# Kernel optimization log

Measured on AMD Instinct MI355X. Metric: run time of the kernel, lower is better.

The kernel has to match this reference:

```python
import jax, jax.numpy as jnp
import numpy as np

B, T, I, H, FF, C = 4096, 512, 13, 7, 512, 1


def setup_inputs() -> dict:
    key = jax.random.key(0)
    ks = jax.random.split(key, 9)
    s_ih = 1.0 / np.sqrt(H)
    return {
        "x": jax.random.normal(ks[0], (B, T, I), dtype=jnp.float32),
        # PyTorch LSTM params, gate order i,f,g,o, uniform(-1/sqrt(H), 1/sqrt(H))
        "w_ih": jax.random.uniform(ks[1], (4 * H, I), minval=-s_ih, maxval=s_ih, dtype=jnp.float32),
        "w_hh": jax.random.uniform(ks[2], (4 * H, H), minval=-s_ih, maxval=s_ih, dtype=jnp.float32),
        "b_ih": jax.random.uniform(ks[3], (4 * H,), minval=-s_ih, maxval=s_ih, dtype=jnp.float32),
        "b_hh": jax.random.uniform(ks[4], (4 * H,), minval=-s_ih, maxval=s_ih, dtype=jnp.float32),
        "fc1_w": jax.random.uniform(ks[5], (FF, H), minval=-s_ih, maxval=s_ih, dtype=jnp.float32),
        "fc1_b": jax.random.uniform(ks[6], (FF,), minval=-s_ih, maxval=s_ih, dtype=jnp.float32),
        "fc_w": jax.random.uniform(ks[7], (C, FF), minval=-1.0 / np.sqrt(FF), maxval=1.0 / np.sqrt(FF), dtype=jnp.float32),
        "fc_b": jax.random.uniform(ks[8], (C,), minval=-1.0 / np.sqrt(FF), maxval=1.0 / np.sqrt(FF), dtype=jnp.float32),
    }


def _lstm_last_hidden(x, w_ih, w_hh, b_ih, b_hh):
    # Precompute input contributions for all timesteps: [B, T, 4H]
    xg = jnp.einsum("bti,gi->btg", x, w_ih) + b_ih

    def step(carry, xg_t):
        h, c = carry
        gates = xg_t + h @ w_hh.T + b_hh  # [B, 4H]
        i, f, g, o = jnp.split(gates, 4, axis=-1)
        i = jax.nn.sigmoid(i)
        f = jax.nn.sigmoid(f)
        g = jnp.tanh(g)
        o = jax.nn.sigmoid(o)
        c = f * c + i * g
        h = o * jnp.tanh(c)
        return (h, c), None

    h0 = jnp.zeros((x.shape[0], w_hh.shape[1]), dtype=x.dtype)
    (hn, _), _ = jax.lax.scan(step, (h0, h0), jnp.swapaxes(xg, 0, 1))
    return hn  # [B, H]


def reference(x, w_ih, w_hh, b_ih, b_hh, fc1_w, fc1_b, fc_w, fc_b):
    # Dropout(0.1) is identity in eval mode.
    hn = _lstm_last_hidden(x, w_ih, w_hh, b_ih, b_hh)
    out = jax.nn.relu(hn)
    out = jax.nn.relu(out @ fc1_w.T + fc1_b)
    return out @ fc_w.T + fc_b  # [B, 1]
```

## Files before the change

kernel.cpp:

```cpp
#include <hip/hip_runtime.h>

#define BB 4096
#define TN 512
#define IN 13
#define HN 7
#define FFD 512
#define CT 16
#define NCK (TN / CT)
#define GPB 2

#define SWZ(v, imm) __int_as_float(__builtin_amdgcn_ds_swizzle(__float_as_int(v), (imm)))
#define QB(v, q)    __int_as_float(__builtin_amdgcn_mov_dpp(__float_as_int(v), (q)*0x55, 0xF, 0xF, true))

__device__ __forceinline__ float2 pkfma(float2 a, float2 b, float2 c) {
    float2 d;
    asm("v_pk_fma_f32 %0, %1, %2, %3" : "=v"(d) : "v"(a), "v"(b), "v"(c));
    return d;
}

__global__ __launch_bounds__(128, 7)
void lstm_fused(const float* __restrict__ x,
                const float* __restrict__ w_ih,
                const float* __restrict__ w_hh,
                const float* __restrict__ b_ih,
                const float* __restrict__ b_hh,
                const float* __restrict__ fc1_w,
                const float* __restrict__ fc1_b,
                const float* __restrict__ fc_w,
                const float* __restrict__ fc_b,
                float* __restrict__ out)
{
    __shared__ float2 xd2[2][CT/2][64];
    __shared__ float  xs[IN][GPB][CT];

    const int tid  = threadIdx.x;
    const int wid  = tid >> 6;
    const int l64  = tid & 63;
    const int grp  = l64 >> 5;
    const int lane = l64 & 31;
    const int b    = blockIdx.x * GPB + grp;

    const int tau = lane & 3;
    const int ju  = lane >> 2;
    const int jj  = (ju < HN) ? ju : (HN - 1);
    const int row = tau * HN + jj;

    const float L2E  = 1.4426950408889634f;
    const bool  is_tanh = (tau == 2);
    const float kmul = is_tanh ? (-2.0f * L2E) : (-L2E);
    const float sc   = is_tanh ?  2.0f : 1.0f;
    const float offc = is_tanh ? -1.0f : 0.0f;

    const int s_st = lane & 15;
    const int h_st = (lane >> 4) & 1;
    const int cb   = h_st * 7;
    float2 w2[IN];
    float2 bias2;
    float  p[7];

    float whh[HN];

    if (wid == 1) {
#pragma unroll
        for (int i = 0; i < IN; ++i) {
            const float w = kmul * w_ih[row * IN + i];
            w2[i] = make_float2(w, w);
        }
        const float bsum = kmul * (b_ih[row] + b_hh[row]);
        bias2 = make_float2(bsum, bsum);
    } else {
#pragma unroll
        for (int k = 0; k < HN; ++k) whh[k] = kmul * w_hh[row * HN + k];
        __builtin_amdgcn_s_setprio(1);
    }

    float h0 = 0.f, h1 = 0.f, h2 = 0.f, h3 = 0.f, h4 = 0.f, h5 = 0.f, h6 = 0.f;
    float cval = 0.0f;

    if (wid == 1) {
        const float* src0 = x + ((long)b * TN + s_st) * IN + cb;
#pragma unroll
        for (int c = 0; c < 6; ++c) p[c] = src0[c];
        if (h_st == 0) p[6] = src0[6];
#pragma unroll
        for (int c = 0; c < 6; ++c) xs[cb + c][grp][s_st] = p[c];
        if (h_st == 0) xs[cb + 6][grp][s_st] = p[6];
        {
            const float* src1 = x + ((long)b * TN + CT + s_st) * IN + cb;
#pragma unroll
            for (int c = 0; c < 6; ++c) p[c] = src1[c];
            if (h_st == 0) p[6] = src1[6];
        }
#pragma unroll
        for (int q = 0; q < CT; q += 4) {
            float2 accA = bias2, accB = bias2;
#pragma unroll
            for (int i = 0; i < IN; ++i) {
                const float4 xv = *(const float4*)&xs[i][grp][q];
                accA = pkfma(w2[i], make_float2(xv.x, xv.y), accA);
                accB = pkfma(w2[i], make_float2(xv.z, xv.w), accB);
            }
            xd2[0][(q >> 1) + 0][l64] = accA;
            xd2[0][(q >> 1) + 1][l64] = accB;
        }
    }
    __syncthreads();

    for (int ck = 0; ck < NCK; ++ck) {
        if (wid == 1) {
            const int nk = ck + 1;
            if (nk < NCK) {
#pragma unroll
                for (int c = 0; c < 6; ++c) xs[cb + c][grp][s_st] = p[c];
                if (h_st == 0) xs[cb + 6][grp][s_st] = p[6];
                if (nk + 1 < NCK) {
                    const float* src = x + ((long)b * TN + (nk + 1) * CT + s_st) * IN + cb;
#pragma unroll
                    for (int c = 0; c < 6; ++c) p[c] = src[c];
                    if (h_st == 0) p[6] = src[6];
                }
                const int buf = nk & 1;
#pragma unroll
                for (int q = 0; q < CT; q += 4) {
                    float2 accA = bias2, accB = bias2;
#pragma unroll
                    for (int i = 0; i < IN; ++i) {
                        const float4 xv = *(const float4*)&xs[i][grp][q];
                        accA = pkfma(w2[i], make_float2(xv.x, xv.y), accA);
                        accB = pkfma(w2[i], make_float2(xv.z, xv.w), accB);
                    }
                    xd2[buf][(q >> 1) + 0][l64] = accA;
                    xd2[buf][(q >> 1) + 1][l64] = accB;
                }
            }
        } else {
            const int buf = ck & 1;
            float xr[CT];
#pragma unroll
            for (int pq = 0; pq < CT / 2; ++pq) {
                const float2 v = xd2[buf][pq][l64];
                xr[2 * pq]     = v.x;
                xr[2 * pq + 1] = v.y;
            }
#pragma unroll
            for (int s = 0; s < CT; ++s) {
                float s0 = fmaf(whh[0], h0, xr[s]);
                s0 = fmaf(whh[1], h1, s0);
                s0 = fmaf(whh[2], h2, s0);
                s0 = fmaf(whh[3], h3, s0);
                float s1 = whh[4] * h4;
                s1 = fmaf(whh[5], h5, s1);
                s1 = fmaf(whh[6], h6, s1);
                const float sg = s0 + s1;

                float e   = __builtin_amdgcn_exp2f(sg);
                float val = fmaf(__builtin_amdgcn_rcpf(1.0f + e), sc, offc);

                const float iv = QB(val, 0);
                const float fv = QB(val, 1);
                const float gv = QB(val, 2);
                const float ov = QB(val, 3);

                cval = fmaf(fv, cval, iv * gv);
                float e2 = __builtin_amdgcn_exp2f(-2.0f * L2E * cval);
                float th = fmaf(__builtin_amdgcn_rcpf(1.0f + e2), 2.0f, -1.0f);
                const float hq = ov * th;

                h0 = SWZ(hq, (0  << 5));
                h1 = SWZ(hq, (4  << 5));
                h2 = SWZ(hq, (8  << 5));
                h3 = SWZ(hq, (12 << 5));
                h4 = SWZ(hq, (16 << 5));
                h5 = SWZ(hq, (20 << 5));
                h6 = SWZ(hq, (24 << 5));
            }
        }
        __syncthreads();
    }

    if (wid == 1) return;

    float hb[HN] = { fmaxf(h0,0.f), fmaxf(h1,0.f), fmaxf(h2,0.f), fmaxf(h3,0.f),
                     fmaxf(h4,0.f), fmaxf(h5,0.f), fmaxf(h6,0.f) };

    float acc = 0.0f;
#pragma unroll
    for (int k = 0; k < FFD / 32; ++k) {
        const int r = lane + (k << 5);
        float s = fc1_b[r];
#pragma unroll
        for (int j = 0; j < HN; ++j) s = fmaf(fc1_w[r * HN + j], hb[j], s);
        s = fmaxf(s, 0.0f);
        acc = fmaf(fc_w[r], s, acc);
    }
#pragma unroll
    for (int o = 16; o >= 1; o >>= 1) acc += __shfl_xor(acc, o, 32);
    if (lane == 0) out[b] = acc + fc_b[0];
}

extern "C" void kernel_launch(void* const* d_in, const int* in_sizes, int n_in,
                              void* d_out, int out_size, void* d_ws, size_t ws_size,
                              hipStream_t stream) {
    const float* x     = (const float*)d_in[0];
    const float* w_ih  = (const float*)d_in[1];
    const float* w_hh  = (const float*)d_in[2];
    const float* b_ih  = (const float*)d_in[3];
    const float* b_hh  = (const float*)d_in[4];
    const float* fc1_w = (const float*)d_in[5];
    const float* fc1_b = (const float*)d_in[6];
    const float* fc_w  = (const float*)d_in[7];
    const float* fc_b  = (const float*)d_in[8];
    float* out = (float*)d_out;

    dim3 grid(BB / GPB);
    dim3 block(128);
    hipLaunchKernelGGL(lstm_fused, grid, block, 0, stream,
                       x, w_ih, w_hh, b_ih, b_hh, fc1_w, fc1_b, fc_w, fc_b, out);
}
```

Before: 105.2 us.

## Replace ds_swizzle hidden-state broadcast with permlane16 swap plus DPP row rotates

The per-step broadcast of the 7 hidden values across lanes moves from seven LDS-crossbar ds_swizzle ops to one v_permlane16_swap and six DPP row_ror moves. The recurrent weights are re-permuted at setup so each lane's rotated operand pairs with the right w_hh column, with zero weights padding the missing 8th slot. This targets the latency of the serial LSTM recurrence, where each step waits on the h exchange. The launch-bounds occupancy hint also drops from 7 to 4, which loosens the register budget but may lower the number of resident waves.

```diff
diff --git a/kernel.cpp b/kernel.cpp
--- a/kernel.cpp
+++ b/kernel.cpp
@@ -9,8 +9,32 @@
 #define NCK (TN / CT)
 #define GPB 2
 
-#define SWZ(v, imm) __int_as_float(__builtin_amdgcn_ds_swizzle(__float_as_int(v), (imm)))
+#if defined(__has_builtin)
+#  if __has_builtin(__builtin_amdgcn_permlane16_swap)
+#    define HAVE_PL16 1
+#  endif
+#endif
+
 #define QB(v, q)    __int_as_float(__builtin_amdgcn_mov_dpp(__float_as_int(v), (q)*0x55, 0xF, 0xF, true))
+#define RORF(v, n)  __int_as_float(__builtin_amdgcn_mov_dpp(__float_as_int(v), 0x120 + (n), 0xF, 0xF, true))
+
+__device__ __forceinline__ void rowswap(float& a, float& b) {
+#ifdef HAVE_PL16
+    auto r = __builtin_amdgcn_permlane16_swap(__float_as_uint(a), __float_as_uint(b),
+                                              false, false);
+    a = __uint_as_float(r[0]);
+    b = __uint_as_float(r[1]);
+#else
+    float ta, tb;
+    asm volatile("v_mov_b32 %0, %2\n"
+                 "v_mov_b32 %1, %3\n"
+                 "s_nop 1\n"
+                 "v_permlane16_swap_b32 %0, %1"
+                 : "=&v"(ta), "=&v"(tb)
+                 : "v"(a), "v"(b));
+    a = ta; b = tb;
+#endif
+}
 
 __device__ __forceinline__ float2 pkfma(float2 a, float2 b, float2 c) {
     float2 d;
@@ -18,7 +42,7 @@
     return d;
 }
 
-__global__ __launch_bounds__(128, 7)
+__global__ __launch_bounds__(128, 4)
 void lstm_fused(const float* __restrict__ x,
                 const float* __restrict__ w_ih,
                 const float* __restrict__ w_hh,
@@ -44,12 +68,21 @@
     const int ju  = lane >> 2;
     const int jj  = (ju < HN) ? ju : (HN - 1);
     const int row = tau * HN + jj;
+    const int jr  = ju & 3;
 
     const float L2E  = 1.4426950408889634f;
     const bool  is_tanh = (tau == 2);
     const float kmul = is_tanh ? (-2.0f * L2E) : (-L2E);
     const float sc   = is_tanh ?  2.0f : 1.0f;
     const float offc = is_tanh ? -1.0f : 0.0f;
+
+    const int pr = __builtin_amdgcn_mov_dpp(l64, 0x124, 0xF, 0xF, true);
+    const bool ror_plus = ((pr & 15) == ((l64 + 4) & 15));
+    float paf = __int_as_float(l64);
+    float pbf = __int_as_float(l64 + 64);
+    rowswap(paf, pbf);
+    const int pa = __float_as_int(paf) & 63;
+    const bool a_even = (((pa >> 4) & 1) == 0);
 
     const int s_st = lane & 15;
     const int h_st = (lane >> 4) & 1;
@@ -58,7 +91,7 @@
     float2 bias2;
     float  p[7];
 
-    float whh[HN];
+    float wA[4], wB[4];
 
     if (wid == 1) {
 #pragma unroll
@@ -70,12 +103,21 @@
         bias2 = make_float2(bsum, bsum);
     } else {
 #pragma unroll
-        for (int k = 0; k < HN; ++k) whh[k] = kmul * w_hh[row * HN + k];
-        __builtin_amdgcn_s_setprio(1);
-    }
-
-    float h0 = 0.f, h1 = 0.f, h2 = 0.f, h3 = 0.f, h4 = 0.f, h5 = 0.f, h6 = 0.f;
+        for (int k = 0; k < 4; ++k) {
+            const int dk  = ror_plus ? k : ((4 - k) & 3);
+            const int cL  = (jr + dk) & 3;
+            const int cH  = 4 + ((jr + dk) & 3);
+            const float wL = kmul * w_hh[row * HN + cL];
+            const float wH = (cH < HN) ? kmul * w_hh[row * HN + cH] : 0.0f;
+            wA[k] = a_even ? wL : wH;
+            wB[k] = a_even ? wH : wL;
+        }
+    }
+
+    float a0 = 0.f, a1 = 0.f, a2 = 0.f, a3 = 0.f;
+    float b0 = 0.f, b1 = 0.f, b2 = 0.f, b3 = 0.f;
     float cval = 0.0f;
+    float hq_final = 0.0f;
 
     if (wid == 1) {
         const float* src0 = x + ((long)b * TN + s_st) * IN + cb;
@@ -144,14 +186,15 @@
             }
 #pragma unroll
             for (int s = 0; s < CT; ++s) {
-                float s0 = fmaf(whh[0], h0, xr[s]);
-                s0 = fmaf(whh[1], h1, s0);
-                s0 = fmaf(whh[2], h2, s0);
-                s0 = fmaf(whh[3], h3, s0);
-                float s1 = whh[4] * h4;
-                s1 = fmaf(whh[5], h5, s1);
-                s1 = fmaf(whh[6], h6, s1);
-                const float sg = s0 + s1;
+                float t0 = fmaf(wA[0], a0, xr[s]);
+                t0 = fmaf(wA[1], a1, t0);
+                t0 = fmaf(wA[2], a2, t0);
+                t0 = fmaf(wA[3], a3, t0);
+                float t1 = wB[0] * b0;
+                t1 = fmaf(wB[1], b1, t1);
+                t1 = fmaf(wB[2], b2, t1);
+                t1 = fmaf(wB[3], b3, t1);
+                const float sg = t0 + t1;
 
                 float e   = __builtin_amdgcn_exp2f(sg);
                 float val = fmaf(__builtin_amdgcn_rcpf(1.0f + e), sc, offc);
@@ -165,14 +208,16 @@
                 float e2 = __builtin_amdgcn_exp2f(-2.0f * L2E * cval);
                 float th = fmaf(__builtin_amdgcn_rcpf(1.0f + e2), 2.0f, -1.0f);
                 const float hq = ov * th;
-
-                h0 = SWZ(hq, (0  << 5));
-                h1 = SWZ(hq, (4  << 5));
-                h2 = SWZ(hq, (8  << 5));
-                h3 = SWZ(hq, (12 << 5));
-                h4 = SWZ(hq, (16 << 5));
-                h5 = SWZ(hq, (20 << 5));
-                h6 = SWZ(hq, (24 << 5));
+                hq_final = hq;
+
+                a0 = hq; b0 = hq;
+                rowswap(a0, b0);
+                a1 = RORF(a0, 4);
+                a2 = RORF(a0, 8);
+                a3 = RORF(a0, 12);
+                b1 = RORF(b0, 4);
+                b2 = RORF(b0, 8);
+                b3 = RORF(b0, 12);
             }
         }
         __syncthreads();
@@ -180,8 +225,9 @@
 
     if (wid == 1) return;
 
-    float hb[HN] = { fmaxf(h0,0.f), fmaxf(h1,0.f), fmaxf(h2,0.f), fmaxf(h3,0.f),
-                     fmaxf(h4,0.f), fmaxf(h5,0.f), fmaxf(h6,0.f) };
+    float hb[HN];
+#pragma unroll
+    for (int j = 0; j < HN; ++j) hb[j] = fmaxf(__shfl(hq_final, 4 * j, 32), 0.0f);
 
     float acc = 0.0f;
 #pragma unroll
```

Measured after the change: 110.7 us. +5.3%, slower.
